# Kernel optimization log

Hardware: AMD Instinct MI355X
Metric: run time of the kernel (lower is better)

The kernel has to match this reference:

```python
import jax, jax.numpy as jnp
import numpy as np
from jax import lax

H = 64          # GRU hidden size
OUT_STEPS = 20  # output_seq_size


def _maxpool2(x):
    # x: [N, C, H, W] -> 2x2 max pool, stride 2, VALID
    return lax.reduce_window(x, -jnp.inf, lax.max, (1, 1, 2, 2), (1, 1, 2, 2), 'VALID')


def _conv(x, w, b):
    # NCHW / OIHW, VALID, stride 1
    y = lax.conv_general_dilated(x, w, (1, 1), 'VALID',
                                 dimension_numbers=('NCHW', 'OIHW', 'NCHW'))
    return y + b[None, :, None, None]


def _gru_step(h, x, wih, whh, bih, bhh):
    # PyTorch GRU gate order: r, z, n
    gi = x @ wih.T + bih            # [B, 3H]
    gh = h @ whh.T + bhh            # [B, 3H]
    i_r, i_z, i_n = jnp.split(gi, 3, axis=-1)
    h_r, h_z, h_n = jnp.split(gh, 3, axis=-1)
    r = jax.nn.sigmoid(i_r + h_r)
    z = jax.nn.sigmoid(i_z + h_z)
    n = jnp.tanh(i_n + r * h_n)
    return (1.0 - z) * n + z * h


def setup_inputs() -> dict:
    key = jax.random.key(0)
    ks = jax.random.split(key, 20)
    B, T = 1024, 31
    s = 0.1
    return {
        'bbox_seq': jax.random.normal(ks[0], (B, T, 4), jnp.float32),
        'head_seq': jax.random.uniform(ks[1], (B, T, 32, 32), jnp.float32),
        'conv1_w': jax.random.normal(ks[2], (4, 1, 3, 3), jnp.float32) * s,
        'conv1_b': jax.random.normal(ks[3], (4,), jnp.float32) * s,
        'conv2_w': jax.random.normal(ks[4], (10, 4, 3, 3), jnp.float32) * s,
        'conv2_b': jax.random.normal(ks[5], (10,), jnp.float32) * s,
        'fc_w': jax.random.normal(ks[6], (5, 360), jnp.float32) * s,
        'fc_b': jax.random.normal(ks[7], (5,), jnp.float32) * s,
        'enc_wih': jax.random.normal(ks[8], (3 * H, 9), jnp.float32) * s,
        'enc_whh': jax.random.normal(ks[9], (3 * H, H), jnp.float32) * s,
        'enc_bih': jax.random.normal(ks[10], (3 * H,), jnp.float32) * s,
        'enc_bhh': jax.random.normal(ks[11], (3 * H,), jnp.float32) * s,
        'dec_wih': jax.random.normal(ks[12], (3 * H, 4), jnp.float32) * s,
        'dec_whh': jax.random.normal(ks[13], (3 * H, H), jnp.float32) * s,
        'dec_bih': jax.random.normal(ks[14], (3 * H,), jnp.float32) * s,
        'dec_bhh': jax.random.normal(ks[15], (3 * H,), jnp.float32) * s,
        'lin_w': jax.random.normal(ks[16], (4, H), jnp.float32) * s,
        'lin_b': jax.random.normal(ks[17], (4,), jnp.float32) * s,
    }


def reference(bbox_seq, head_seq, conv1_w, conv1_b, conv2_w, conv2_b, fc_w, fc_b,
              enc_wih, enc_whh, enc_bih, enc_bhh,
              dec_wih, dec_whh, dec_bih, dec_bhh, lin_w, lin_b):
    B, T = bbox_seq.shape[0], bbox_seq.shape[1]
    L = T - 1  # encoder sequence length

    # offset: last bbox, broadcast over OUT_STEPS -> [B, OUT_STEPS, 4]
    offset = jnp.broadcast_to(bbox_seq[:, -1][:, None, :], (B, OUT_STEPS, 4))

    diffs = bbox_seq[:, 1:] - bbox_seq[:, :-1]  # [B, L, 4] (dropout p=0 -> identity)

    # --- ConvEncoder on all head crops at once ---
    imgs = head_seq[:, :-1].reshape(B * L, 1, 32, 32)
    x = jax.nn.relu(_conv(imgs, conv1_w, conv1_b))   # [BL, 4, 30, 30]
    x = _maxpool2(x)                                  # [BL, 4, 15, 15]
    x = jax.nn.relu(_conv(x, conv2_w, conv2_b))       # [BL, 10, 13, 13]
    x = _maxpool2(x)                                  # [BL, 10, 6, 6]
    emb = x.reshape(B * L, -1) @ fc_w.T + fc_b        # [BL, 5]
    emb = emb.reshape(B, L, -1)

    enc_in = jnp.concatenate([diffs, emb], axis=2)    # [B, L, 9]

    # --- GRU encoder (scan over time) ---
    def enc_step(h, x_t):
        h = _gru_step(h, x_t, enc_wih, enc_whh, enc_bih, enc_bhh)
        return h, None
    h0 = jnp.zeros((B, H), enc_in.dtype)
    hn, _ = lax.scan(enc_step, h0, jnp.swapaxes(enc_in, 0, 1))

    def dec_step(carry, _):
        h, prev_x = carry
        h = _gru_step(h, prev_x, dec_wih, dec_whh, dec_bih, dec_bhh)
        x_new = h @ lin_w.T + lin_b + prev_x
        return (h, x_new), x_new
    (_, _), outs = lax.scan(dec_step, (hn, diffs[:, -1]), None, length=OUT_STEPS)
    out = jnp.swapaxes(outs, 0, 1)                    # [B, OUT_STEPS, 4]

    return jnp.cumsum(out, axis=1) + offset
```

## Files before the change

kernel.cpp:

```cpp
#include <hip/hip_runtime.h>
#include <hip/hip_bf16.h>


#define B_      1024
#define L_      30
#define H_      64
#define NGRUBLK 64

typedef _Float16 half_t;
typedef __attribute__((ext_vector_type(8))) _Float16 half8;
typedef __attribute__((ext_vector_type(4))) float f32x4;

#define MFMA16(A, B, C) __builtin_amdgcn_mfma_f32_16x16x32_f16(A, B, C, 0, 0, 0)

__device__ __forceinline__ float sigmoid_f(float v) {
    return __builtin_amdgcn_rcpf(1.f + __expf(-v));
}
__device__ __forceinline__ float tanh_f(float v) {
    v = fminf(fmaxf(v, -15.f), 15.f);
    const float e = __expf(2.f * v);
    return (e - 1.f) * __builtin_amdgcn_rcpf(e + 1.f);
}
__device__ __forceinline__ void load4_lds(float* r, const float* p) {
    float2 a = *(const float2*)p;
    float2 b = *(const float2*)(p + 2);
    r[0] = a.x; r[1] = a.y; r[2] = b.x; r[3] = b.y;
}

union alignas(16) SharedU {
    struct {
        half_t hbuf[2][16][72];
        half_t xenc[16][40];
        half_t xdec[16][40];
    } g;
    struct {
        float s_img[32 * 32];
        float s_p1[4 * 15 * 16];
        float s_p2[360];
        float s_red[60];
    } c[4];
};

__global__ __launch_bounds__(256, 3) void fused_kernel(
    const float* __restrict__ bbox,
    const float* __restrict__ head,
    const float* __restrict__ c1w, const float* __restrict__ c1b,
    const float* __restrict__ c2w, const float* __restrict__ c2b,
    const float* __restrict__ fcw, const float* __restrict__ fcb,
    const float* __restrict__ ewih, const float* __restrict__ ewhh,
    const float* __restrict__ ebih, const float* __restrict__ ebhh,
    const float* __restrict__ dwih, const float* __restrict__ dwhh,
    const float* __restrict__ dbih, const float* __restrict__ dbhh,
    const float* __restrict__ linw, const float* __restrict__ linb,
    float* __restrict__ enc_in,
    unsigned*            flags,
    float* __restrict__ out)
{
    __shared__ SharedU su;
    const int tid = threadIdx.x;

    if (blockIdx.x >= NGRUBLK) {
        const int cb   = (int)blockIdx.x - NGRUBLK;
        const int sub  = tid >> 6;
        const int lane = tid & 63;
        const int img  = (cb << 2) | sub;
        const int ts   = img >> 10;
        const int b    = img & 1023;
        auto& S = su.c[sub];

        {
            const float4* src = (const float4*)(head + ((size_t)b * 31 + (size_t)ts) * 1024);
            float4* dstv = (float4*)S.s_img;
            #pragma unroll
            for (int i = 0; i < 4; ++i) dstv[lane + 64 * i] = src[lane + 64 * i];
        }
        __syncthreads();

        if (lane < 60) {
            const int c = lane / 15, px = lane % 15;
            const int x0 = 2 * px;
            float wg[9];
            #pragma unroll
            for (int k = 0; k < 9; ++k) wg[k] = c1w[c * 9 + k];
            const float bias = c1b[c];

            auto c1out = [&](const float* ra, const float* rb, const float* rc, const float* rd) -> float {
                float a00 = bias, a01 = bias, a10 = bias, a11 = bias;
                #pragma unroll
                for (int kx = 0; kx < 3; ++kx) {
                    const float w0 = wg[kx], w1 = wg[3 + kx], w2 = wg[6 + kx];
                    a00 = fmaf(w0, ra[kx],     fmaf(w1, rb[kx],     fmaf(w2, rc[kx],     a00)));
                    a01 = fmaf(w0, ra[kx + 1], fmaf(w1, rb[kx + 1], fmaf(w2, rc[kx + 1], a01)));
                    a10 = fmaf(w0, rb[kx],     fmaf(w1, rc[kx],     fmaf(w2, rd[kx],     a10)));
                    a11 = fmaf(w0, rb[kx + 1], fmaf(w1, rc[kx + 1], fmaf(w2, rd[kx + 1], a11)));
                }
                a00 = fmaxf(a00, 0.f); a01 = fmaxf(a01, 0.f);
                a10 = fmaxf(a10, 0.f); a11 = fmaxf(a11, 0.f);
                return fmaxf(fmaxf(a00, a01), fmaxf(a10, a11));
            };

            float r[6][4];
            load4_lds(r[0], S.s_img + 0 * 32 + x0);
            load4_lds(r[1], S.s_img + 1 * 32 + x0);
            #pragma unroll
            for (int i = 0; i < 7; ++i) {
                const int s0 = (4 * i) % 6, s1 = (4 * i + 1) % 6, s2 = (4 * i + 2) % 6;
                const int s3 = (4 * i + 3) % 6, s4 = (4 * i + 4) % 6, s5 = (4 * i + 5) % 6;
                load4_lds(r[s2], S.s_img + (4 * i + 2) * 32 + x0);
                load4_lds(r[s3], S.s_img + (4 * i + 3) * 32 + x0);
                S.s_p1[c * 240 + (2 * i) * 16 + px] = c1out(r[s0], r[s1], r[s2], r[s3]);
                load4_lds(r[s4], S.s_img + (4 * i + 4) * 32 + x0);
                load4_lds(r[s5], S.s_img + (4 * i + 5) * 32 + x0);
                S.s_p1[c * 240 + (2 * i + 1) * 16 + px] = c1out(r[s2], r[s3], r[s4], r[s5]);
            }
            load4_lds(r[0], S.s_img + 30 * 32 + x0);
            load4_lds(r[1], S.s_img + 31 * 32 + x0);
            S.s_p1[c * 240 + 14 * 16 + px] = c1out(r[4], r[5], r[0], r[1]);
        }
        __syncthreads();

        if (lane < 60) {
            const int c = lane / 6, px = lane % 6;
            const int x0 = 2 * px;
            float wg2[4][9];
            #pragma unroll
            for (int ic = 0; ic < 4; ++ic)
                #pragma unroll
                for (int k = 0; k < 9; ++k) wg2[ic][k] = c2w[(c * 4 + ic) * 9 + k];
            const float bias2 = c2b[c];

            float P[6][4][4];
            auto c2out = [&](float (*pa)[4], float (*pb)[4], float (*pc)[4], float (*pd)[4]) -> float {
                float a00 = bias2, a01 = bias2, a10 = bias2, a11 = bias2;
                #pragma unroll
                for (int ic = 0; ic < 4; ++ic) {
                    #pragma unroll
                    for (int kx = 0; kx < 3; ++kx) {
                        const float w0 = wg2[ic][kx], w1 = wg2[ic][3 + kx], w2 = wg2[ic][6 + kx];
                        a00 = fmaf(w0, pa[ic][kx],     fmaf(w1, pb[ic][kx],     fmaf(w2, pc[ic][kx],     a00)));
                        a01 = fmaf(w0, pa[ic][kx + 1], fmaf(w1, pb[ic][kx + 1], fmaf(w2, pc[ic][kx + 1], a01)));
                        a10 = fmaf(w0, pb[ic][kx],     fmaf(w1, pc[ic][kx],     fmaf(w2, pd[ic][kx],     a10)));
                        a11 = fmaf(w0, pb[ic][kx + 1], fmaf(w1, pc[ic][kx + 1], fmaf(w2, pd[ic][kx + 1], a11)));
                    }
                }
                a00 = fmaxf(a00, 0.f); a01 = fmaxf(a01, 0.f);
                a10 = fmaxf(a10, 0.f); a11 = fmaxf(a11, 0.f);
                return fmaxf(fmaxf(a00, a01), fmaxf(a10, a11));
            };

            #pragma unroll
            for (int ic = 0; ic < 4; ++ic) {
                load4_lds(P[0][ic], S.s_p1 + ic * 240 + 0 * 16 + x0);
                load4_lds(P[1][ic], S.s_p1 + ic * 240 + 1 * 16 + x0);
            }
            #pragma unroll
            for (int i = 0; i < 3; ++i) {
                const int s0 = (4 * i) % 6, s1 = (4 * i + 1) % 6, s2 = (4 * i + 2) % 6;
                const int s3 = (4 * i + 3) % 6, s4 = (4 * i + 4) % 6, s5 = (4 * i + 5) % 6;
                #pragma unroll
                for (int ic = 0; ic < 4; ++ic) {
                    load4_lds(P[s2][ic], S.s_p1 + ic * 240 + (4 * i + 2) * 16 + x0);
                    load4_lds(P[s3][ic], S.s_p1 + ic * 240 + (4 * i + 3) * 16 + x0);
                }
                S.s_p2[c * 36 + (2 * i) * 6 + px] = c2out(P[s0], P[s1], P[s2], P[s3]);
                #pragma unroll
                for (int ic = 0; ic < 4; ++ic) {
                    load4_lds(P[s4][ic], S.s_p1 + ic * 240 + (4 * i + 4) * 16 + x0);
                    load4_lds(P[s5][ic], S.s_p1 + ic * 240 + (4 * i + 5) * 16 + x0);
                }
                S.s_p2[c * 36 + (2 * i + 1) * 6 + px] = c2out(P[s2], P[s3], P[s4], P[s5]);
            }
        }
        __syncthreads();

        if (lane < 60) {
            const int o = lane / 12, i0 = lane % 12;
            const float* wrow = fcw + o * 360;
            float acc = 0.f;
            #pragma unroll
            for (int k = 0; k < 30; ++k) {
                const int i = i0 + 12 * k;
                acc = fmaf(wrow[i], S.s_p2[i], acc);
            }
            S.s_red[lane] = acc;
        }
        __syncthreads();

        float* dst = enc_in + ((size_t)b * L_ + ts) * 9;
        if (lane < 5) {
            float acc = fcb[lane];
            #pragma unroll
            for (int k = 0; k < 12; ++k) acc += S.s_red[lane * 12 + k];
            __hip_atomic_store(&dst[4 + lane], acc, __ATOMIC_RELAXED, __HIP_MEMORY_SCOPE_AGENT);
        } else if (lane >= 8 && lane < 12) {
            const int d = lane - 8;
            const float* bbp = bbox + (size_t)b * 124 + (size_t)ts * 4;
            __hip_atomic_store(&dst[d], bbp[4 + d] - bbp[d], __ATOMIC_RELAXED, __HIP_MEMORY_SCOPE_AGENT);
        }
        __syncthreads();
        if (tid == 0)
            __hip_atomic_store(&flags[cb], 1u, __ATOMIC_RELAXED, __HIP_MEMORY_SCOPE_AGENT);
        return;
    }

    const int g   = (int)blockIdx.x;
    const int bb  = g * 16;
    const int w   = tid >> 6;
    const int l   = tid & 63;
    const int q   = l >> 4;
    const int col = l & 15;
    auto& G = su.g;

    {
        int4* p = (int4*)&G;
        #pragma unroll
        for (int i = 0; i < 2; ++i) {
            const int idx = tid + 256 * i;
            if (idx < (int)(sizeof(G) / 16)) p[idx] = int4{0, 0, 0, 0};
        }
    }

    const int urow = 16 * w + col;
    auto whh_frag = [&](const float* W, int gate, int kap) -> half8 {
        const float* rp = W + (size_t)(gate * 64 + urow) * 64 + kap * 32 + q * 8;
        half8 f;
        #pragma unroll
        for (int j = 0; j < 8; ++j) f[j] = (half_t)rp[j];
        return f;
    };
    auto wih_frag = [&](const float* W, int gate, int indim) -> half8 {
        half8 f;
        #pragma unroll
        for (int j = 0; j < 8; ++j) {
            const int d = q * 8 + j;
            f[j] = (d < indim) ? (half_t)W[(size_t)(gate * 64 + urow) * indim + d]
                               : (half_t)0.f;
        }
        return f;
    };

    const half8 eBr0 = whh_frag(ewhh, 0, 0), eBr1 = whh_frag(ewhh, 0, 1);
    const half8 eBz0 = whh_frag(ewhh, 1, 0), eBz1 = whh_frag(ewhh, 1, 1);
    const half8 eBn0 = whh_frag(ewhh, 2, 0), eBn1 = whh_frag(ewhh, 2, 1);
    const half8 eBrx = wih_frag(ewih, 0, 9);
    const half8 eBzx = wih_frag(ewih, 1, 9);
    const half8 eBnx = wih_frag(ewih, 2, 9);

    const float ebr  = ebih[urow]       + ebhh[urow];
    const float ebz  = ebih[64 + urow]  + ebhh[64 + urow];
    const float ebnh = ebhh[128 + urow];
    const float ebni = ebih[128 + urow];

    float hold[4] = {0.f, 0.f, 0.f, 0.f};
    __syncthreads();

    for (int t = 0; t < L_; ++t) {
        if (tid < 4) {
            const unsigned fidx = (unsigned)(t * 256 + 4 * g + tid);
            while (__hip_atomic_load(&flags[fidx], __ATOMIC_RELAXED,
                                     __HIP_MEMORY_SCOPE_AGENT) == 0u)
                __builtin_amdgcn_s_sleep(2);
        }
        __syncthreads();
        if (tid < 144) {
            const int bq = tid / 9, d = tid - 9 * bq;
            const float v = __hip_atomic_load(
                &enc_in[((size_t)(bb + bq) * L_ + t) * 9 + d],
                __ATOMIC_RELAXED, __HIP_MEMORY_SCOPE_AGENT);
            G.xenc[bq][d] = (half_t)v;
        }
        __syncthreads();

        const int p = t & 1;
        const half8 a0 = *(const half8*)&G.hbuf[p][col][q * 8];
        const half8 a1 = *(const half8*)&G.hbuf[p][col][32 + q * 8];
        const half8 a2 = *(const half8*)&G.xenc[col][q * 8];

        f32x4 Cr  = {ebr, ebr, ebr, ebr};
        f32x4 Cz  = {ebz, ebz, ebz, ebz};
        f32x4 Cnh = {ebnh, ebnh, ebnh, ebnh};
        f32x4 Cnx = {ebni, ebni, ebni, ebni};
        Cr  = MFMA16(a0, eBr0, Cr);  Cr  = MFMA16(a1, eBr1, Cr);  Cr = MFMA16(a2, eBrx, Cr);
        Cz  = MFMA16(a0, eBz0, Cz);  Cz  = MFMA16(a1, eBz1, Cz);  Cz = MFMA16(a2, eBzx, Cz);
        Cnh = MFMA16(a0, eBn0, Cnh); Cnh = MFMA16(a1, eBn1, Cnh);
        Cnx = MFMA16(a2, eBnx, Cnx);

        #pragma unroll
        for (int r = 0; r < 4; ++r) {
            const float rr = sigmoid_f(Cr[r]);
            const float zz = sigmoid_f(Cz[r]);
            const float nn = tanh_f(Cnx[r] + rr * Cnh[r]);
            hold[r] = fmaf(zz, hold[r] - nn, nn);
            G.hbuf[p ^ 1][q * 4 + r][urow] = (half_t)hold[r];
        }
        __syncthreads();
    }

    const half8 dBr0 = whh_frag(dwhh, 0, 0), dBr1 = whh_frag(dwhh, 0, 1);
    const half8 dBz0 = whh_frag(dwhh, 1, 0), dBz1 = whh_frag(dwhh, 1, 1);
    const half8 dBn0 = whh_frag(dwhh, 2, 0), dBn1 = whh_frag(dwhh, 2, 1);
    const half8 dBrx = wih_frag(dwih, 0, 4);
    const half8 dBzx = wih_frag(dwih, 1, 4);
    const half8 dBnx = wih_frag(dwih, 2, 4);

    half8 Bl0, Bl1;
    #pragma unroll
    for (int j = 0; j < 8; ++j) {
        Bl0[j] = (col < 4) ? (half_t)linw[col * 64 +      q * 8 + j] : (half_t)0.f;
        Bl1[j] = (col < 4) ? (half_t)linw[col * 64 + 32 + q * 8 + j] : (half_t)0.f;
    }

    const float dbr  = dbih[urow]       + dbhh[urow];
    const float dbz  = dbih[64 + urow]  + dbhh[64 + urow];
    const float dbnh = dbhh[128 + urow];
    const float dbni = dbih[128 + urow];
    const float lb   = (col < 4) ? linb[col] : 0.f;

    float xold[4], ofs[4], cs[4];
    if (w == 0 && col < 4) {
        #pragma unroll
        for (int r = 0; r < 4; ++r) {
            const float* bbp = bbox + (size_t)(bb + q * 4 + r) * 124;
            xold[r] = bbp[120 + col] - bbp[116 + col];
            ofs[r]  = bbp[120 + col];
            cs[r]   = 0.f;
            G.xdec[q * 4 + r][col] = (half_t)xold[r];
        }
    }
    __syncthreads();

    for (int tt = 0; tt < 20; ++tt) {
        const int p = tt & 1;
        const half8 a0 = *(const half8*)&G.hbuf[p][col][q * 8];
        const half8 a1 = *(const half8*)&G.hbuf[p][col][32 + q * 8];
        const half8 a2 = *(const half8*)&G.xdec[col][q * 8];

        f32x4 Cr  = {dbr, dbr, dbr, dbr};
        f32x4 Cz  = {dbz, dbz, dbz, dbz};
        f32x4 Cnh = {dbnh, dbnh, dbnh, dbnh};
        f32x4 Cnx = {dbni, dbni, dbni, dbni};
        Cr  = MFMA16(a0, dBr0, Cr);  Cr  = MFMA16(a1, dBr1, Cr);  Cr = MFMA16(a2, dBrx, Cr);
        Cz  = MFMA16(a0, dBz0, Cz);  Cz  = MFMA16(a1, dBz1, Cz);  Cz = MFMA16(a2, dBzx, Cz);
        Cnh = MFMA16(a0, dBn0, Cnh); Cnh = MFMA16(a1, dBn1, Cnh);
        Cnx = MFMA16(a2, dBnx, Cnx);

        #pragma unroll
        for (int r = 0; r < 4; ++r) {
            const float rr = sigmoid_f(Cr[r]);
            const float zz = sigmoid_f(Cz[r]);
            const float nn = tanh_f(Cnx[r] + rr * Cnh[r]);
            hold[r] = fmaf(zz, hold[r] - nn, nn);
            G.hbuf[p ^ 1][q * 4 + r][urow] = (half_t)hold[r];
        }
        __syncthreads();

        const half8 al0 = *(const half8*)&G.hbuf[p ^ 1][col][q * 8];
        const half8 al1 = *(const half8*)&G.hbuf[p ^ 1][col][32 + q * 8];
        f32x4 X = {0.f, 0.f, 0.f, 0.f};
        X = MFMA16(al0, Bl0, X);
        X = MFMA16(al1, Bl1, X);

        if (w == 0 && col < 4) {
            #pragma unroll
            for (int r = 0; r < 4; ++r) {
                const float xv = X[r] + lb + xold[r];
                xold[r] = xv;
                cs[r] += xv;
                G.xdec[q * 4 + r][col] = (half_t)xv;
                out[(size_t)(bb + q * 4 + r) * 80 + tt * 4 + col] = cs[r] + ofs[r];
            }
        }
        __syncthreads();
    }
}

extern "C" void kernel_launch(void* const* d_in, const int* in_sizes, int n_in,
                              void* d_out, int out_size, void* d_ws, size_t ws_size,
                              hipStream_t stream) {
    (void)in_sizes; (void)n_in; (void)out_size; (void)ws_size;
    const float* bbox = (const float*)d_in[0];
    const float* head = (const float*)d_in[1];
    const float* c1w  = (const float*)d_in[2];
    const float* c1b  = (const float*)d_in[3];
    const float* c2w  = (const float*)d_in[4];
    const float* c2b  = (const float*)d_in[5];
    const float* fcw  = (const float*)d_in[6];
    const float* fcb  = (const float*)d_in[7];
    const float* ewih = (const float*)d_in[8];
    const float* ewhh = (const float*)d_in[9];
    const float* ebih = (const float*)d_in[10];
    const float* ebhh = (const float*)d_in[11];
    const float* dwih = (const float*)d_in[12];
    const float* dwhh = (const float*)d_in[13];
    const float* dbih = (const float*)d_in[14];
    const float* dbhh = (const float*)d_in[15];
    const float* linw = (const float*)d_in[16];
    const float* linb = (const float*)d_in[17];
    float* out = (float*)d_out;

    float*    enc_in = (float*)d_ws;
    unsigned* flags  = (unsigned*)((char*)d_ws + (size_t)B_ * L_ * 9 * sizeof(float));

    hipMemsetAsync(flags, 0, (B_ * L_ / 4) * sizeof(unsigned), stream);

    const int grid = NGRUBLK + (B_ * L_) / 4;
    fused_kernel<<<grid, 256, 0, stream>>>(bbox, head, c1w, c1b, c2w, c2b,
                                           fcw, fcb, ewih, ewhh, ebih, ebhh,
                                           dwih, dwhh, dbih, dbhh, linw, linb,
                                           enc_in, flags, out);
}
```

Baseline: 275.4 us.

## Compute conv2 with fp16 MFMA implicit GEMM and shrink conv shared memory

The second convolution now runs as an implicit GEMM on MFMA 16x16x32 fp16 instructions instead of scalar FMAs. Conv1 output is stored as channel-interleaved fp16 so that each lane can load contiguous K slices. The full 13x13 conv2 map is written to LDS, reusing the image buffer, and a separate pass does the 2x2 max pool. The smaller LDS footprint lets launch bounds rise to 4 blocks per CU, at the cost of fp16 rounding of intermediate activations and an extra sync and pool pass.

Result: slower. 306.9 us (+11.4%).

```diff
diff --git a/kernel.cpp b/kernel.cpp
--- a/kernel.cpp
+++ b/kernel.cpp
@@ -8,6 +8,8 @@
 #define NGRUBLK 64
 
 typedef _Float16 half_t;
+typedef __attribute__((ext_vector_type(2))) _Float16 half2_t;
+typedef __attribute__((ext_vector_type(4))) _Float16 half4;
 typedef __attribute__((ext_vector_type(8))) _Float16 half8;
 typedef __attribute__((ext_vector_type(4))) float f32x4;
 
@@ -27,21 +29,26 @@
     r[0] = a.x; r[1] = a.y; r[2] = b.x; r[3] = b.y;
 }
 
+struct alignas(16) ConvSub {
+    union {
+        float  s_img[32 * 32];
+        half_t c2h[2048];
+    } u;
+    half_t s_p1h[15 * 64];
+    float  s_p2[360];
+    float  s_red[60];
+};
+
 union alignas(16) SharedU {
     struct {
         half_t hbuf[2][16][72];
         half_t xenc[16][40];
         half_t xdec[16][40];
     } g;
-    struct {
-        float s_img[32 * 32];
-        float s_p1[4 * 15 * 16];
-        float s_p2[360];
-        float s_red[60];
-    } c[4];
+    ConvSub c[4];
 };
 
-__global__ __launch_bounds__(256, 3) void fused_kernel(
+__global__ __launch_bounds__(256, 4) void fused_kernel(
     const float* __restrict__ bbox,
     const float* __restrict__ head,
     const float* __restrict__ c1w, const float* __restrict__ c1b,
@@ -68,9 +75,24 @@
         const int b    = img & 1023;
         auto& S = su.c[sub];
 
+        const int oc = lane & 15;
+        const int q  = lane >> 4;
+        half8 B1, B2;
+        #pragma unroll
+        for (int j = 0; j < 8; ++j) {
+            const int slot = ((q & 1) << 3) | j;
+            const int kx = slot >> 2, ic = slot & 3;
+            const int ky1 = q >> 1;
+            B1[j] = (oc < 10 && kx < 3)
+                  ? (half_t)c2w[oc * 36 + ic * 9 + ky1 * 3 + kx] : (half_t)0.f;
+            B2[j] = (oc < 10 && kx < 3 && q < 2)
+                  ? (half_t)c2w[oc * 36 + ic * 9 + 6 + kx] : (half_t)0.f;
+        }
+        const float bc2 = (oc < 10) ? c2b[oc] : 0.f;
+
         {
             const float4* src = (const float4*)(head + ((size_t)b * 31 + (size_t)ts) * 1024);
-            float4* dstv = (float4*)S.s_img;
+            float4* dstv = (float4*)S.u.s_img;
             #pragma unroll
             for (int i = 0; i < 4; ++i) dstv[lane + 64 * i] = src[lane + 64 * i];
         }
@@ -100,75 +122,78 @@
             };
 
             float r[6][4];
-            load4_lds(r[0], S.s_img + 0 * 32 + x0);
-            load4_lds(r[1], S.s_img + 1 * 32 + x0);
+            load4_lds(r[0], S.u.s_img + 0 * 32 + x0);
+            load4_lds(r[1], S.u.s_img + 1 * 32 + x0);
             #pragma unroll
             for (int i = 0; i < 7; ++i) {
                 const int s0 = (4 * i) % 6, s1 = (4 * i + 1) % 6, s2 = (4 * i + 2) % 6;
                 const int s3 = (4 * i + 3) % 6, s4 = (4 * i + 4) % 6, s5 = (4 * i + 5) % 6;
-                load4_lds(r[s2], S.s_img + (4 * i + 2) * 32 + x0);
-                load4_lds(r[s3], S.s_img + (4 * i + 3) * 32 + x0);
-                S.s_p1[c * 240 + (2 * i) * 16 + px] = c1out(r[s0], r[s1], r[s2], r[s3]);
-                load4_lds(r[s4], S.s_img + (4 * i + 4) * 32 + x0);
-                load4_lds(r[s5], S.s_img + (4 * i + 5) * 32 + x0);
-                S.s_p1[c * 240 + (2 * i + 1) * 16 + px] = c1out(r[s2], r[s3], r[s4], r[s5]);
+                load4_lds(r[s2], S.u.s_img + (4 * i + 2) * 32 + x0);
+                load4_lds(r[s3], S.u.s_img + (4 * i + 3) * 32 + x0);
+                S.s_p1h[(2 * i) * 64 + px * 4 + c] = (half_t)c1out(r[s0], r[s1], r[s2], r[s3]);
+                load4_lds(r[s4], S.u.s_img + (4 * i + 4) * 32 + x0);
+                load4_lds(r[s5], S.u.s_img + (4 * i + 5) * 32 + x0);
+                S.s_p1h[(2 * i + 1) * 64 + px * 4 + c] = (half_t)c1out(r[s2], r[s3], r[s4], r[s5]);
             }
-            load4_lds(r[0], S.s_img + 30 * 32 + x0);
-            load4_lds(r[1], S.s_img + 31 * 32 + x0);
-            S.s_p1[c * 240 + 14 * 16 + px] = c1out(r[4], r[5], r[0], r[1]);
-        }
-        __syncthreads();
-
-        if (lane < 60) {
-            const int c = lane / 6, px = lane % 6;
-            const int x0 = 2 * px;
-            float wg2[4][9];
-            #pragma unroll
-            for (int ic = 0; ic < 4; ++ic)
+            load4_lds(r[0], S.u.s_img + 30 * 32 + x0);
+            load4_lds(r[1], S.u.s_img + 31 * 32 + x0);
+            S.s_p1h[14 * 64 + px * 4 + c] = (half_t)c1out(r[4], r[5], r[0], r[1]);
+
+            S.s_p1h[(lane % 15) * 64 + 60 + lane / 15] = (half_t)0.f;
+        }
+        __syncthreads();
+
+        {
+            const int m = lane & 15;
+            const int off = (q & 1) << 3;
+            #pragma unroll
+            for (int t2 = 0; t2 < 11; ++t2) {
+                const int pm0 = t2 * 16 + m;
+                const int pm  = pm0 > 168 ? 168 : pm0;
+                const int py  = (pm * 79) >> 10;
+                const int px  = pm - py * 13;
+                const int base1 = (py + (q >> 1)) * 64 + px * 4 + off;
+                const int base2 = (py + 2) * 64 + px * 4 + off;
+                const half4 a1lo = *(const half4*)&S.s_p1h[base1];
+                const half4 a1hi = *(const half4*)&S.s_p1h[base1 + 4];
+                const half4 a2lo = *(const half4*)&S.s_p1h[base2];
+                const half4 a2hi = *(const half4*)&S.s_p1h[base2 + 4];
+                half8 a1, a2;
                 #pragma unroll
-                for (int k = 0; k < 9; ++k) wg2[ic][k] = c2w[(c * 4 + ic) * 9 + k];
-            const float bias2 = c2b[c];
-
-            float P[6][4][4];
-            auto c2out = [&](float (*pa)[4], float (*pb)[4], float (*pc)[4], float (*pd)[4]) -> float {
-                float a00 = bias2, a01 = bias2, a10 = bias2, a11 = bias2;
-                #pragma unroll
-                for (int ic = 0; ic < 4; ++ic) {
+                for (int j = 0; j < 4; ++j) {
+                    a1[j] = a1lo[j]; a1[4 + j] = a1hi[j];
+                    a2[j] = a2lo[j]; a2[4 + j] = a2hi[j];
+                }
+                f32x4 Cc = {bc2, bc2, bc2, bc2};
+                Cc = MFMA16(a1, B1, Cc);
+                Cc = MFMA16(a2, B2, Cc);
+
+                if (oc < 10) {
                     #pragma unroll
-                    for (int kx = 0; kx < 3; ++kx) {
-                        const float w0 = wg2[ic][kx], w1 = wg2[ic][3 + kx], w2 = wg2[ic][6 + kx];
-                        a00 = fmaf(w0, pa[ic][kx],     fmaf(w1, pb[ic][kx],     fmaf(w2, pc[ic][kx],     a00)));
-                        a01 = fmaf(w0, pa[ic][kx + 1], fmaf(w1, pb[ic][kx + 1], fmaf(w2, pc[ic][kx + 1], a01)));
-                        a10 = fmaf(w0, pb[ic][kx],     fmaf(w1, pc[ic][kx],     fmaf(w2, pd[ic][kx],     a10)));
-                        a11 = fmaf(w0, pb[ic][kx + 1], fmaf(w1, pc[ic][kx + 1], fmaf(w2, pd[ic][kx + 1], a11)));
+                    for (int r2 = 0; r2 < 4; ++r2) {
+                        const int p = t2 * 16 + q * 4 + r2;
+                        if (p < 169) {
+                            const int wy = (p * 79) >> 10;
+                            const int wx = p - wy * 13;
+                            S.u.c2h[oc * 182 + wy * 14 + wx] =
+                                (half_t)fmaxf(Cc[r2], 0.f);
+                        }
                     }
                 }
-                a00 = fmaxf(a00, 0.f); a01 = fmaxf(a01, 0.f);
-                a10 = fmaxf(a10, 0.f); a11 = fmaxf(a11, 0.f);
-                return fmaxf(fmaxf(a00, a01), fmaxf(a10, a11));
-            };
-
-            #pragma unroll
-            for (int ic = 0; ic < 4; ++ic) {
-                load4_lds(P[0][ic], S.s_p1 + ic * 240 + 0 * 16 + x0);
-                load4_lds(P[1][ic], S.s_p1 + ic * 240 + 1 * 16 + x0);
             }
-            #pragma unroll
-            for (int i = 0; i < 3; ++i) {
-                const int s0 = (4 * i) % 6, s1 = (4 * i + 1) % 6, s2 = (4 * i + 2) % 6;
-                const int s3 = (4 * i + 3) % 6, s4 = (4 * i + 4) % 6, s5 = (4 * i + 5) % 6;
-                #pragma unroll
-                for (int ic = 0; ic < 4; ++ic) {
-                    load4_lds(P[s2][ic], S.s_p1 + ic * 240 + (4 * i + 2) * 16 + x0);
-                    load4_lds(P[s3][ic], S.s_p1 + ic * 240 + (4 * i + 3) * 16 + x0);
-                }
-                S.s_p2[c * 36 + (2 * i) * 6 + px] = c2out(P[s0], P[s1], P[s2], P[s3]);
-                #pragma unroll
-                for (int ic = 0; ic < 4; ++ic) {
-                    load4_lds(P[s4][ic], S.s_p1 + ic * 240 + (4 * i + 4) * 16 + x0);
-                    load4_lds(P[s5][ic], S.s_p1 + ic * 240 + (4 * i + 5) * 16 + x0);
-                }
-                S.s_p2[c * 36 + (2 * i + 1) * 6 + px] = c2out(P[s2], P[s3], P[s4], P[s5]);
+        }
+        __syncthreads();
+
+        if (lane < 60) {
+            const int c = lane / 6, x = lane % 6;
+            const half_t* cbase = &S.u.c2h[c * 182 + 2 * x];
+            float* dstp = &S.s_p2[c * 36 + x];
+            #pragma unroll
+            for (int y = 0; y < 6; ++y) {
+                const half2_t ha = *(const half2_t*)(cbase + (2 * y) * 14);
+                const half2_t hb = *(const half2_t*)(cbase + (2 * y + 1) * 14);
+                dstp[y * 6] = fmaxf(fmaxf((float)ha[0], (float)ha[1]),
+                                    fmaxf((float)hb[0], (float)hb[1]));
             }
         }
         __syncthreads();
```
